# Kernel tuning notes

Hardware: AMD Instinct MI355X
Metric: run time of the kernel (lower is better)

The kernel has to match this reference:

```python
import jax, jax.numpy as jnp
import numpy as np

N, IN_C, HID, E = 100000, 1024, 128, 1600000


def setup_inputs() -> dict:
    key = jax.random.key(0)
    k1, k2, k3 = jax.random.split(key, 3)
    x = jax.random.normal(k1, (N, IN_C), dtype=jnp.float32)
    # GCNConv weight (bias=False), applied as x @ W : [in, hidden]
    W = jax.random.normal(k2, (IN_C, HID), dtype=jnp.float32) * (1.0 / np.sqrt(IN_C))
    edge_index = jax.random.randint(k3, (2, E), 0, N, dtype=jnp.int64)
    return {"x": x, "W": W, "edge_index": edge_index}


def reference(x, W, edge_index):
    n = x.shape[0]
    row, col = edge_index[0], edge_index[1]  # src -> dst
    # add self-loops (PyG GCNConv default)
    loop = jnp.arange(n, dtype=edge_index.dtype)
    row = jnp.concatenate([row, loop])
    col = jnp.concatenate([col, loop])
    # symmetric normalization: deg on destination, includes self-loops (deg >= 1)
    deg = jax.ops.segment_sum(jnp.ones(col.shape, jnp.float32), col, num_segments=n)
    dinv = jax.lax.rsqrt(deg)
    norm = dinv[row] * dinv[col]  # [E+N]
    # linear transform first (in -> hidden), then gather/scale/scatter-add
    h = x @ W                      # [N, HID]
    msg = h[row] * norm[:, None]   # [E+N, HID]
    out = jax.ops.segment_sum(msg, col, num_segments=n)  # [N, HID]
    return out
```

## Files before the change

kernel.cpp:

```cpp
#include <hip/hip_runtime.h>
#include <hip/hip_bf16.h>

#define NN 100000
#define INC 1024
#define HID 128
#define NE 1600000
#define NB ((NN + 255) / 256)

typedef float floatx4 __attribute__((ext_vector_type(4)));
typedef __bf16 bf16x8 __attribute__((ext_vector_type(8)));
typedef unsigned short ushort8v __attribute__((ext_vector_type(8)));
typedef unsigned short ushort4v __attribute__((ext_vector_type(4)));

__device__ __forceinline__ unsigned short f2bf(float f) {
    union { float f; unsigned u; } v; v.f = f;
    unsigned r = v.u + 0x7fffu + ((v.u >> 16) & 1u);
    return (unsigned short)(r >> 16);
}

__device__ __forceinline__ float bf_lo(unsigned u) {
    union { unsigned u; float f; } v; v.u = u << 16; return v.f;
}
__device__ __forceinline__ float bf_hi(unsigned u) {
    union { unsigned u; float f; } v; v.u = u & 0xffff0000u; return v.f;
}

__global__ __launch_bounds__(256) void init_k(int* cnt, const float* __restrict__ W,
                                              unsigned short* __restrict__ Wt) {
    const int b = blockIdx.x;
    if (b < NB) {
        const int i = b * 256 + threadIdx.x;
        if (i < NN) cnt[i] = 0;
    } else {
        const int idx = (b - NB) * 256 + threadIdx.x;
        const int n = idx >> 10, k = idx & 1023;
        Wt[idx] = f2bf(W[k * HID + n]);
    }
}

__global__ __launch_bounds__(256) void deg_edges_k(const int* __restrict__ col, int* cnt) {
    int e = blockIdx.x * 256 + threadIdx.x;
    if (e < NE) atomicAdd(&cnt[col[e]], 1);
}

__global__ __launch_bounds__(256) void scan1_k(const int* __restrict__ cnt,
                                               int* __restrict__ excl, int* __restrict__ bsum,
                                               float* __restrict__ dinv) {
    __shared__ int sh[256];
    const int t = threadIdx.x, b = blockIdx.x;
    const int idx = b * 256 + t;
    const int v = (idx < NN) ? cnt[idx] : 0;
    sh[t] = v;
    __syncthreads();
#pragma unroll
    for (int off = 1; off < 256; off <<= 1) {
        const int x = sh[t];
        const int y = (t >= off) ? sh[t - off] : 0;
        __syncthreads();
        sh[t] = x + y;
        __syncthreads();
    }
    if (idx < NN) {
        excl[idx] = sh[t] - v;
        dinv[idx] = rsqrtf((float)(v + 1));
    }
    if (t == 255) bsum[b] = sh[255];
}

__global__ __launch_bounds__(512) void scan2_k(const int* __restrict__ bsum, int* __restrict__ boff) {
    __shared__ int sh[512];
    const int t = threadIdx.x;
    const int v = (t < NB) ? bsum[t] : 0;
    sh[t] = v;
    __syncthreads();
#pragma unroll
    for (int off = 1; off < 512; off <<= 1) {
        const int x = sh[t];
        const int y = (t >= off) ? sh[t - off] : 0;
        __syncthreads();
        sh[t] = x + y;
        __syncthreads();
    }
    if (t < NB) boff[t] = sh[t] - v;
}

__global__ __launch_bounds__(256) void scan3_k(const int* __restrict__ excl, const int* __restrict__ boff,
                                               int* __restrict__ rowptr, int* __restrict__ cursor) {
    const int idx = blockIdx.x * 256 + threadIdx.x;
    if (idx < NN) {
        const int v = excl[idx] + boff[blockIdx.x];
        rowptr[idx] = v;
        cursor[idx] = v;
    }
    if (idx == 0) rowptr[NN] = NE;
}

__global__ __launch_bounds__(256) void fill_k(const int* __restrict__ ei,
                                              int* cursor, int* __restrict__ ssrc) {
    const int e = blockIdx.x * 256 + threadIdx.x;
    if (e < NE) {
        const int r = ei[e];
        const int c = ei[NE + e];
        const int pos = atomicAdd(&cursor[c], 1);
        ssrc[pos] = r;
    }
}

__global__ __launch_bounds__(256) void gemm_hp_k(
    const float* __restrict__ x, const unsigned short* __restrict__ Wt,
    const float* __restrict__ dinv, unsigned short* __restrict__ hp)
{
    __shared__ unsigned short As[2][64 * 40];
    __shared__ unsigned short Bs[2][128 * 40];
    const int tid  = threadIdx.x;
    const int lane = tid & 63;
    const int wave = tid >> 6;
    const int q    = lane >> 4;
    const int l16  = lane & 15;
    const int brow = blockIdx.x * 64;

    const int am  = tid >> 3;
    const int akk = (tid & 7) * 4;
    const int bn  = tid >> 1;
    const int bkk = (tid & 1) * 16;

    floatx4 acc[8];
#pragma unroll
    for (int t = 0; t < 8; ++t) acc[t] = (floatx4){0.f, 0.f, 0.f, 0.f};

    float4   va[2];
    ushort8v vb[2];

    {
#pragma unroll
        for (int h = 0; h < 2; ++h) {
            const int g = brow + am + h * 32;
            float4 v = make_float4(0.f, 0.f, 0.f, 0.f);
            if (g < NN) v = *(const float4*)&x[(size_t)g * INC + akk];
            va[h] = v;
        }
        vb[0] = *(const ushort8v*)&Wt[(size_t)bn * INC + bkk];
        vb[1] = *(const ushort8v*)&Wt[(size_t)bn * INC + bkk + 8];
    }

    int buf = 0;
    for (int k0 = 0; k0 < INC; k0 += 32) {
        {
#pragma unroll
            for (int h = 0; h < 2; ++h) {
                ushort4v w;
                w.x = f2bf(va[h].x); w.y = f2bf(va[h].y);
                w.z = f2bf(va[h].z); w.w = f2bf(va[h].w);
                *(ushort4v*)&As[buf][(am + h * 32) * 40 + akk] = w;
            }
            *(ushort8v*)&Bs[buf][bn * 40 + bkk]     = vb[0];
            *(ushort8v*)&Bs[buf][bn * 40 + bkk + 8] = vb[1];
        }
        __syncthreads();

        const int kn = k0 + 32;
        if (kn < INC) {
#pragma unroll
            for (int h = 0; h < 2; ++h) {
                const int g = brow + am + h * 32;
                float4 v = make_float4(0.f, 0.f, 0.f, 0.f);
                if (g < NN) v = *(const float4*)&x[(size_t)g * INC + kn + akk];
                va[h] = v;
            }
            vb[0] = *(const ushort8v*)&Wt[(size_t)bn * INC + kn + bkk];
            vb[1] = *(const ushort8v*)&Wt[(size_t)bn * INC + kn + bkk + 8];
        }

        const bf16x8 af = *(const bf16x8*)&As[buf][(wave * 16 + l16) * 40 + q * 8];
#pragma unroll
        for (int t = 0; t < 8; ++t) {
            const bf16x8 bfv = *(const bf16x8*)&Bs[buf][(t * 16 + l16) * 40 + q * 8];
            acc[t] = __builtin_amdgcn_mfma_f32_16x16x32_bf16(af, bfv, acc[t], 0, 0, 0);
        }
        buf ^= 1;
    }

#pragma unroll
    for (int r = 0; r < 4; ++r) {
        const int row = brow + wave * 16 + q * 4 + r;
        if (row < NN) {
            const float d = dinv[row];
#pragma unroll
            for (int t = 0; t < 8; ++t) {
                const int col = t * 16 + l16;
                hp[(size_t)row * HID + col] = f2bf(acc[t][r] * d);
            }
        }
    }
}

__global__ __launch_bounds__(256) void agg_k(const int* __restrict__ rowptr,
                                             const int* __restrict__ ssrc,
                                             const unsigned short* __restrict__ hp,
                                             const float* __restrict__ dinv,
                                             float* __restrict__ out)
{
    const int w = (blockIdx.x * 256 + threadIdx.x) >> 6;
    const int lane = threadIdx.x & 63;
    if (w >= NN) return;
    const int s = rowptr[w];
    const int e = rowptr[w + 1];
    const unsigned* hp32 = (const unsigned*)hp;

    const unsigned uself = hp32[(size_t)w * 64 + lane];
    float ax = bf_lo(uself), ay = bf_hi(uself);

    for (int i = s; i < e; i += 64) {
        const int rem = e - i;
        const int cnt = rem < 64 ? rem : 64;
        int srcv = 0;
        if (lane < rem) srcv = ssrc[i + lane];
        int j = 0;
        for (; j + 4 <= cnt; j += 4) {
            const int s0 = __shfl(srcv, j + 0);
            const int s1 = __shfl(srcv, j + 1);
            const int s2 = __shfl(srcv, j + 2);
            const int s3 = __shfl(srcv, j + 3);
            const unsigned v0 = hp32[(size_t)s0 * 64 + lane];
            const unsigned v1 = hp32[(size_t)s1 * 64 + lane];
            const unsigned v2 = hp32[(size_t)s2 * 64 + lane];
            const unsigned v3 = hp32[(size_t)s3 * 64 + lane];
            ax += bf_lo(v0) + bf_lo(v1) + bf_lo(v2) + bf_lo(v3);
            ay += bf_hi(v0) + bf_hi(v1) + bf_hi(v2) + bf_hi(v3);
        }
        for (; j < cnt; ++j) {
            const int sj = __shfl(srcv, j);
            const unsigned v = hp32[(size_t)sj * 64 + lane];
            ax += bf_lo(v);
            ay += bf_hi(v);
        }
    }

    const float d = dinv[w];
    float2 r;
    r.x = ax * d;
    r.y = ay * d;
    *(float2*)&out[(size_t)w * HID + (size_t)lane * 2] = r;
}

extern "C" void kernel_launch(void* const* d_in, const int* in_sizes, int n_in,
                              void* d_out, int out_size, void* d_ws, size_t ws_size,
                              hipStream_t stream) {
    const float* x  = (const float*)d_in[0];
    const float* W  = (const float*)d_in[1];
    const int*   ei = (const int*)d_in[2];
    float* out = (float*)d_out;

    char* p = (char*)d_ws;
    unsigned short* hp = (unsigned short*)p; p += (size_t)NN * HID * 2;
    int*   cnt     = (int*)p;              p += (size_t)NN * 4;
    int*   rowptr  = (int*)p;              p += (size_t)(NN + 4) * 4;
    int*   cursor  = (int*)p;              p += (size_t)NN * 4;
    int*   excl    = (int*)p;              p += (size_t)NN * 4;
    float* dinv    = (float*)p;            p += (size_t)NN * 4;
    unsigned short* Wt = (unsigned short*)p; p += (size_t)INC * HID * 2;
    int*   bsum    = (int*)p;              p += 512 * 4;
    int*   boff    = (int*)p;              p += 512 * 4;
    int*   ssrc    = (int*)p;              p += (size_t)NE * 4;

    init_k     <<<NB + (INC * HID) / 256, 256, 0, stream>>>(cnt, W, Wt);
    deg_edges_k<<<(NE + 255) / 256, 256, 0, stream>>>(ei + NE, cnt);
    scan1_k    <<<NB, 256, 0, stream>>>(cnt, excl, bsum, dinv);
    scan2_k    <<<1, 512, 0, stream>>>(bsum, boff);
    scan3_k    <<<NB, 256, 0, stream>>>(excl, boff, rowptr, cursor);
    fill_k     <<<(NE + 255) / 256, 256, 0, stream>>>(ei, cursor, ssrc);
    gemm_hp_k  <<<(NN + 63) / 64, 256, 0, stream>>>(x, Wt, dinv, hp);
    agg_k      <<<(NN * 64 + 255) / 256, 256, 0, stream>>>(rowptr, ssrc, hp, dinv, out);
}
```

Baseline: 849.3 us.

## Enlarge GEMM row tile to 128 and use scalar index loads in aggregation

The GEMM block now covers 128 rows instead of 64, with each wave computing two 16-row MFMA fragments that share the same B-fragment loads from LDS. This halves how often W is reloaded per row and improves MFMA-to-load ratio, at the cost of more accumulator registers. The aggregation kernel replaces the per-64 index load plus shuffles with scalar readfirstlane loads of neighbor indices and unrolls by 8, so more row gathers are in flight. The GEMM is likely memory-bound on reading x, so the GEMM gain may be limited.

After: 857.0 us. No clear change (+0.9%).

```diff
diff --git a/kernel.cpp b/kernel.cpp
--- a/kernel.cpp
+++ b/kernel.cpp
@@ -110,85 +110,93 @@
     const float* __restrict__ x, const unsigned short* __restrict__ Wt,
     const float* __restrict__ dinv, unsigned short* __restrict__ hp)
 {
-    __shared__ unsigned short As[2][64 * 40];
+    __shared__ unsigned short As[2][128 * 40];
     __shared__ unsigned short Bs[2][128 * 40];
     const int tid  = threadIdx.x;
     const int lane = tid & 63;
     const int wave = tid >> 6;
     const int q    = lane >> 4;
     const int l16  = lane & 15;
-    const int brow = blockIdx.x * 64;
-
-    const int am  = tid >> 3;
-    const int akk = (tid & 7) * 4;
-    const int bn  = tid >> 1;
-    const int bkk = (tid & 1) * 16;
-
-    floatx4 acc[8];
-#pragma unroll
-    for (int t = 0; t < 8; ++t) acc[t] = (floatx4){0.f, 0.f, 0.f, 0.f};
-
-    float4   va[2];
+    const int brow = blockIdx.x * 128;
+
+    const int srow = tid >> 1;
+    const int skk  = (tid & 1) * 16;
+
+    floatx4 acc[2][8];
+#pragma unroll
+    for (int f = 0; f < 2; ++f)
+#pragma unroll
+        for (int t = 0; t < 8; ++t) acc[f][t] = (floatx4){0.f, 0.f, 0.f, 0.f};
+
+    float4   va[4];
     ushort8v vb[2];
 
+    const int ag = brow + srow;
+    const bool aok = (ag < NN);
+    const float* __restrict__ xrow = x + (size_t)ag * INC + skk;
+    const unsigned short* __restrict__ wrow = Wt + (size_t)srow * INC + skk;
+
     {
 #pragma unroll
-        for (int h = 0; h < 2; ++h) {
-            const int g = brow + am + h * 32;
+        for (int j = 0; j < 4; ++j) {
             float4 v = make_float4(0.f, 0.f, 0.f, 0.f);
-            if (g < NN) v = *(const float4*)&x[(size_t)g * INC + akk];
-            va[h] = v;
-        }
-        vb[0] = *(const ushort8v*)&Wt[(size_t)bn * INC + bkk];
-        vb[1] = *(const ushort8v*)&Wt[(size_t)bn * INC + bkk + 8];
+            if (aok) v = *(const float4*)&xrow[4 * j];
+            va[j] = v;
+        }
+        vb[0] = *(const ushort8v*)&wrow[0];
+        vb[1] = *(const ushort8v*)&wrow[8];
     }
 
     int buf = 0;
     for (int k0 = 0; k0 < INC; k0 += 32) {
         {
-#pragma unroll
-            for (int h = 0; h < 2; ++h) {
-                ushort4v w;
-                w.x = f2bf(va[h].x); w.y = f2bf(va[h].y);
-                w.z = f2bf(va[h].z); w.w = f2bf(va[h].w);
-                *(ushort4v*)&As[buf][(am + h * 32) * 40 + akk] = w;
-            }
-            *(ushort8v*)&Bs[buf][bn * 40 + bkk]     = vb[0];
-            *(ushort8v*)&Bs[buf][bn * 40 + bkk + 8] = vb[1];
+            ushort8v w0, w1;
+            w0[0] = f2bf(va[0].x); w0[1] = f2bf(va[0].y); w0[2] = f2bf(va[0].z); w0[3] = f2bf(va[0].w);
+            w0[4] = f2bf(va[1].x); w0[5] = f2bf(va[1].y); w0[6] = f2bf(va[1].z); w0[7] = f2bf(va[1].w);
+            w1[0] = f2bf(va[2].x); w1[1] = f2bf(va[2].y); w1[2] = f2bf(va[2].z); w1[3] = f2bf(va[2].w);
+            w1[4] = f2bf(va[3].x); w1[5] = f2bf(va[3].y); w1[6] = f2bf(va[3].z); w1[7] = f2bf(va[3].w);
+            *(ushort8v*)&As[buf][srow * 40 + skk]     = w0;
+            *(ushort8v*)&As[buf][srow * 40 + skk + 8] = w1;
+            *(ushort8v*)&Bs[buf][srow * 40 + skk]     = vb[0];
+            *(ushort8v*)&Bs[buf][srow * 40 + skk + 8] = vb[1];
         }
         __syncthreads();
 
         const int kn = k0 + 32;
         if (kn < INC) {
 #pragma unroll
-            for (int h = 0; h < 2; ++h) {
-                const int g = brow + am + h * 32;
+            for (int j = 0; j < 4; ++j) {
                 float4 v = make_float4(0.f, 0.f, 0.f, 0.f);
-                if (g < NN) v = *(const float4*)&x[(size_t)g * INC + kn + akk];
-                va[h] = v;
+                if (aok) v = *(const float4*)&xrow[kn + 4 * j];
+                va[j] = v;
             }
-            vb[0] = *(const ushort8v*)&Wt[(size_t)bn * INC + kn + bkk];
-            vb[1] = *(const ushort8v*)&Wt[(size_t)bn * INC + kn + bkk + 8];
-        }
-
-        const bf16x8 af = *(const bf16x8*)&As[buf][(wave * 16 + l16) * 40 + q * 8];
+            vb[0] = *(const ushort8v*)&wrow[kn];
+            vb[1] = *(const ushort8v*)&wrow[kn + 8];
+        }
+
+        const bf16x8 af0 = *(const bf16x8*)&As[buf][(wave * 32 + l16) * 40 + q * 8];
+        const bf16x8 af1 = *(const bf16x8*)&As[buf][(wave * 32 + 16 + l16) * 40 + q * 8];
 #pragma unroll
         for (int t = 0; t < 8; ++t) {
             const bf16x8 bfv = *(const bf16x8*)&Bs[buf][(t * 16 + l16) * 40 + q * 8];
-            acc[t] = __builtin_amdgcn_mfma_f32_16x16x32_bf16(af, bfv, acc[t], 0, 0, 0);
+            acc[0][t] = __builtin_amdgcn_mfma_f32_16x16x32_bf16(af0, bfv, acc[0][t], 0, 0, 0);
+            acc[1][t] = __builtin_amdgcn_mfma_f32_16x16x32_bf16(af1, bfv, acc[1][t], 0, 0, 0);
         }
         buf ^= 1;
     }
 
 #pragma unroll
-    for (int r = 0; r < 4; ++r) {
-        const int row = brow + wave * 16 + q * 4 + r;
-        if (row < NN) {
-            const float d = dinv[row];
-#pragma unroll
-            for (int t = 0; t < 8; ++t) {
-                const int col = t * 16 + l16;
-                hp[(size_t)row * HID + col] = f2bf(acc[t][r] * d);
+    for (int f = 0; f < 2; ++f) {
+#pragma unroll
+        for (int r = 0; r < 4; ++r) {
+            const int row = brow + wave * 32 + f * 16 + q * 4 + r;
+            if (row < NN) {
+                const float d = dinv[row];
+#pragma unroll
+                for (int t = 0; t < 8; ++t) {
+                    const int col = t * 16 + l16;
+                    hp[(size_t)row * HID + col] = f2bf(acc[f][t][r] * d);
+                }
             }
         }
     }
@@ -203,37 +211,41 @@
     const int w = (blockIdx.x * 256 + threadIdx.x) >> 6;
     const int lane = threadIdx.x & 63;
     if (w >= NN) return;
-    const int s = rowptr[w];
-    const int e = rowptr[w + 1];
-    const unsigned* hp32 = (const unsigned*)hp;
+    const int s = __builtin_amdgcn_readfirstlane(rowptr[w]);
+    const int e = __builtin_amdgcn_readfirstlane(rowptr[w + 1]);
+    const unsigned* __restrict__ hp32 = (const unsigned*)hp;
 
     const unsigned uself = hp32[(size_t)w * 64 + lane];
     float ax = bf_lo(uself), ay = bf_hi(uself);
 
-    for (int i = s; i < e; i += 64) {
-        const int rem = e - i;
-        const int cnt = rem < 64 ? rem : 64;
-        int srcv = 0;
-        if (lane < rem) srcv = ssrc[i + lane];
-        int j = 0;
-        for (; j + 4 <= cnt; j += 4) {
-            const int s0 = __shfl(srcv, j + 0);
-            const int s1 = __shfl(srcv, j + 1);
-            const int s2 = __shfl(srcv, j + 2);
-            const int s3 = __shfl(srcv, j + 3);
-            const unsigned v0 = hp32[(size_t)s0 * 64 + lane];
-            const unsigned v1 = hp32[(size_t)s1 * 64 + lane];
-            const unsigned v2 = hp32[(size_t)s2 * 64 + lane];
-            const unsigned v3 = hp32[(size_t)s3 * 64 + lane];
-            ax += bf_lo(v0) + bf_lo(v1) + bf_lo(v2) + bf_lo(v3);
-            ay += bf_hi(v0) + bf_hi(v1) + bf_hi(v2) + bf_hi(v3);
-        }
-        for (; j < cnt; ++j) {
-            const int sj = __shfl(srcv, j);
-            const unsigned v = hp32[(size_t)sj * 64 + lane];
-            ax += bf_lo(v);
-            ay += bf_hi(v);
-        }
+    int i = s;
+    for (; i + 8 <= e; i += 8) {
+        const int s0 = __builtin_amdgcn_readfirstlane(ssrc[i + 0]);
+        const int s1 = __builtin_amdgcn_readfirstlane(ssrc[i + 1]);
+        const int s2 = __builtin_amdgcn_readfirstlane(ssrc[i + 2]);
+        const int s3 = __builtin_amdgcn_readfirstlane(ssrc[i + 3]);
+        const int s4 = __builtin_amdgcn_readfirstlane(ssrc[i + 4]);
+        const int s5 = __builtin_amdgcn_readfirstlane(ssrc[i + 5]);
+        const int s6 = __builtin_amdgcn_readfirstlane(ssrc[i + 6]);
+        const int s7 = __builtin_amdgcn_readfirstlane(ssrc[i + 7]);
+        const unsigned v0 = hp32[(size_t)s0 * 64 + lane];
+        const unsigned v1 = hp32[(size_t)s1 * 64 + lane];
+        const unsigned v2 = hp32[(size_t)s2 * 64 + lane];
+        const unsigned v3 = hp32[(size_t)s3 * 64 + lane];
+        const unsigned v4 = hp32[(size_t)s4 * 64 + lane];
+        const unsigned v5 = hp32[(size_t)s5 * 64 + lane];
+        const unsigned v6 = hp32[(size_t)s6 * 64 + lane];
+        const unsigned v7 = hp32[(size_t)s7 * 64 + lane];
+        ax += bf_lo(v0) + bf_lo(v1) + bf_lo(v2) + bf_lo(v3)
+            + bf_lo(v4) + bf_lo(v5) + bf_lo(v6) + bf_lo(v7);
+        ay += bf_hi(v0) + bf_hi(v1) + bf_hi(v2) + bf_hi(v3)
+            + bf_hi(v4) + bf_hi(v5) + bf_hi(v6) + bf_hi(v7);
+    }
+    for (; i < e; ++i) {
+        const int sj = __builtin_amdgcn_readfirstlane(ssrc[i]);
+        const unsigned v = hp32[(size_t)sj * 64 + lane];
+        ax += bf_lo(v);
+        ay += bf_hi(v);
     }
 
     const float d = dinv[w];
@@ -269,6 +281,6 @@
     scan2_k    <<<1, 512, 0, stream>>>(bsum, boff);
     scan3_k    <<<NB, 256, 0, stream>>>(excl, boff, rowptr, cursor);
     fill_k     <<<(NE + 255) / 256, 256, 0, stream>>>(ei, cursor, ssrc);
-    gemm_hp_k  <<<(NN + 63) / 64, 256, 0, stream>>>(x, Wt, dinv, hp);
+    gemm_hp_k  <<<(NN + 127) / 128, 256, 0, stream>>>(x, Wt, dinv, hp);
     agg_k      <<<(NN * 64 + 255) / 256, 256, 0, stream>>>(rowptr, ssrc, hp, dinv, out);
 }
```
